# Kernel optimization log

Measured on AMD Instinct MI355X. Metric: run time of the kernel, lower is better.

The kernel has to match this reference:

```python
import math
import jax, jax.numpy as jnp
import numpy as np

N = 65536   # total nodes across episodes
H = 512     # hidden size
B = 4096    # number of episodes / decoding items
M = 32      # max neighbors (padded ragged valid_actions)


def setup_inputs() -> dict:
    key = jax.random.key(0)
    ks = jax.random.split(key, 9)
    s = 1.0 / math.sqrt(H)
    return {
        "h_static": jax.random.normal(ks[0], (N, H), jnp.float32),
        "h_dynamic": jax.random.normal(ks[1], (N, H), jnp.float32),
        "Ws_kvl": jax.random.normal(ks[2], (H, 3 * H), jnp.float32) * s,
        "Wd_kvl": jax.random.normal(ks[3], (H, 3 * H), jnp.float32) * s,
        "Wq": jax.random.normal(ks[4], (H, H), jnp.float32) * s,
        "batch": jax.random.randint(ks[5], (N,), 0, B, jnp.int32),
        "current_nodes": jax.random.randint(ks[6], (B,), 0, N),
        "neigh_idx": jax.random.randint(ks[7], (B, M), 0, N),
        "lengths": jax.random.randint(ks[8], (B,), 0, M + 1),
    }


def reference(h_static, h_dynamic, Ws_kvl, Wd_kvl, Wq, batch, current_nodes, neigh_idx, lengths):
    # precompute(): static KVL projection (full 3H GEMM then chunk, as in torch)
    kvl_s = h_static @ Ws_kvl            # [N, 3H]
    K_s = kvl_s[:, :H]
    # forward_batch(): dynamic projection
    kvl_d = h_dynamic @ Wd_kvl           # [N, 3H]
    K_d = kvl_d[:, :H]
    K = K_s + K_d                        # [N, H]  (V is computed but unused for outputs)
    q = (h_static[current_nodes] + h_dynamic[current_nodes]) @ Wq  # [B, H]

    # padded ragged neighbor attention (replaces the Python loop over B)
    Kn = K[neigh_idx]                                        # [B, M, H]
    compat = jnp.einsum('bmh,bh->bm', Kn, q) / math.sqrt(H)  # [B, M]
    mask = jnp.arange(M)[None, :] < lengths[:, None]         # [B, M]
    NEG = jnp.float32(-1e9)
    logits = jnp.where(mask, compat, NEG)

    # categorical sampling via Gumbel-max (Categorical(logits).sample())
    u = jax.random.uniform(jax.random.key(1), (B, M), jnp.float32, 1e-8, 1.0)
    g = -jnp.log(-jnp.log(u))
    idx = jnp.argmax(logits + g, axis=-1)                    # [B]

    logp = jax.nn.log_softmax(logits, axis=-1)               # [B, M]
    lp = jnp.take_along_axis(logp, idx[:, None], axis=1)[:, 0]
    actions = jnp.take_along_axis(neigh_idx, idx[:, None], axis=1)[:, 0]

    # empty neighbor list -> stay at current node, log_prob 0 (matches torch branch)
    nonempty = lengths > 0
    actions = jnp.where(nonempty, actions, current_nodes)
    lp = jnp.where(nonempty, lp, jnp.float32(0.0))
    return actions, lp
```

## Files before the change

### kernel.cpp

```cpp
#include <hip/hip_runtime.h>
#include <cstdint>
#include <cstddef>

#define HDIM 512
#define NM 32
#define NBATCH 4096
#define NNODE 65536
#define CAP 16

typedef float v4f __attribute__((ext_vector_type(4)));

__device__ __forceinline__ unsigned rotl32(unsigned x, unsigned d) {
  return (x << d) | (x >> (32u - d));
}

__device__ __forceinline__ void threefry2x32(unsigned& x0, unsigned& x1) {
  const unsigned ks0 = 0u, ks1 = 1u, ks2 = 0x1BD11BDBu;
  x0 += ks0; x1 += ks1;
#define TF_RND(r) { x0 += x1; x1 = rotl32(x1, (r)); x1 ^= x0; }
  TF_RND(13) TF_RND(15) TF_RND(26) TF_RND(6)
  x0 += ks1; x1 += ks2 + 1u;
  TF_RND(17) TF_RND(29) TF_RND(16) TF_RND(24)
  x0 += ks2; x1 += ks0 + 2u;
  TF_RND(13) TF_RND(15) TF_RND(26) TF_RND(6)
  x0 += ks0; x1 += ks1 + 3u;
  TF_RND(17) TF_RND(29) TF_RND(16) TF_RND(24)
  x0 += ks1; x1 += ks2 + 4u;
  TF_RND(13) TF_RND(15) TF_RND(26) TF_RND(6)
  x0 += ks2; x1 += ks0 + 5u;
#undef TF_RND
}

__global__ __launch_bounds__(256) void zero_cnt(int* __restrict__ cnt,
                                                int* __restrict__ ovf_cnt) {
  const int t = blockIdx.x * 256 + threadIdx.x;
  ((int4*)cnt)[t] = make_int4(0, 0, 0, 0);
  if (t == 0) *ovf_cnt = 0;
}

__global__ __launch_bounds__(256) void b1_and_index(
    const float* __restrict__ Ws, const float* __restrict__ Wd,
    const float* __restrict__ Wq, float* __restrict__ M2T,
    const int* __restrict__ neigh, const int* __restrict__ lens,
    int* __restrict__ cnt, int* __restrict__ bucket,
    int* __restrict__ ovf_cnt, int* __restrict__ ovf_list) {
  const int bid = blockIdx.x;
  const int tid = threadIdx.x;
  if (bid >= 512) {
    const int t = (bid - 512) * 256 + tid;
    const int b = t >> 5, m = t & 31;
    if (m < lens[b]) {
      const int n = neigh[t];
      const int slot = atomicAdd(&cnt[n], 1);
      if (slot < CAP) bucket[n * CAP + slot] = t;
      else { const int o = atomicAdd(ovf_cnt, 1); ovf_list[o] = t; }
    }
    return;
  }
  constexpr int BK = 32, LDT = 36;
  __shared__ float Ast[BK][LDT];
  __shared__ float Bst[BK][LDT];
  const int rt = bid >> 4;
  const int ct = bid & 15;
  const int row0 = rt * 32;
  const int col0 = ct * 32;
  const float* Abase = (row0 < 512) ? Ws : Wd;
  const int arow0 = (row0 < 512) ? row0 : row0 - 512;
  const int tx = tid & 15, ty = tid >> 4;
  const int lr = tid >> 3;
  const int lc = (tid & 7) * 4;
  float acc[2][2] = {};
  for (int k0 = 0; k0 < 512; k0 += BK) {
    const float4 va = *(const float4*)(Abase + (size_t)(arow0 + lr) * 1536 + k0 + lc);
    const float4 vb = *(const float4*)(Wq + (size_t)(col0 + lr) * 512 + k0 + lc);
    Ast[lc + 0][lr] = va.x; Ast[lc + 1][lr] = va.y;
    Ast[lc + 2][lr] = va.z; Ast[lc + 3][lr] = va.w;
    Bst[lc + 0][lr] = vb.x; Bst[lc + 1][lr] = vb.y;
    Bst[lc + 2][lr] = vb.z; Bst[lc + 3][lr] = vb.w;
    __syncthreads();
#pragma unroll
    for (int k = 0; k < BK; ++k) {
      const float a0 = Ast[k][ty * 2], a1 = Ast[k][ty * 2 + 1];
      const float b0 = Bst[k][tx * 2], b1 = Bst[k][tx * 2 + 1];
      acc[0][0] += a0 * b0; acc[0][1] += a0 * b1;
      acc[1][0] += a1 * b0; acc[1][1] += a1 * b1;
    }
    __syncthreads();
  }
#pragma unroll
  for (int i = 0; i < 2; ++i) {
    float2 o;
    o.x = acc[i][0]; o.y = acc[i][1];
    *(float2*)(M2T + (size_t)(row0 + ty * 2 + i) * 512 + col0 + tx * 2) = o;
  }
}

__global__ __launch_bounds__(256) void gemm_v(const float* __restrict__ hs,
                                              const float* __restrict__ hd,
                                              const int* __restrict__ cur,
                                              const float* __restrict__ Bm,
                                              float* __restrict__ C) {
  __shared__ __align__(16) char smem[51200];
  float* As = (float*)smem;
  float* Bs = (float*)(smem + 33792);
  float* mg = (float*)smem;

  const int tid = threadIdx.x;
  const int team = tid >> 7;
  const int lt = tid & 127;
  const int swz = (blockIdx.x & 7) * 64 + (blockIdx.x >> 3);
  const int row0 = (swz >> 4) * 128;
  const int col0 = (swz & 15) * 64;
  const int tx = tid & 7;
  const int ty = (tid >> 3) & 15;
  const int r0 = lt >> 3;
  const int cq = (lt & 7) * 4;
  const int kb = team * 256;
  const int aoff = team * 4224;
  const int boff = team * 2176;

  size_t na[8];
#pragma unroll
  for (int p = 0; p < 8; ++p)
    na[p] = (size_t)cur[row0 + r0 + 16 * p] * HDIM + kb + cq;
  const float* bbase = Bm + (size_t)(col0 + r0) * 512 + kb + cq;

  float acc[8][8] = {};
#pragma unroll 1
  for (int t = 0; t < 8; ++t) {
    const int k0 = t * 32;
    float4 va[8], vd[8], vb[4];
#pragma unroll
    for (int p = 0; p < 8; ++p) {
      va[p] = *(const float4*)(hs + na[p] + k0);
      vd[p] = *(const float4*)(hd + na[p] + k0);
    }
#pragma unroll
    for (int p = 0; p < 4; ++p)
      vb[p] = *(const float4*)(bbase + p * (16 * 512) + k0);
    __syncthreads();
#pragma unroll
    for (int p = 0; p < 8; ++p) {
      const int r = r0 + 16 * p;
      As[aoff + (cq + 0) * 132 + r] = va[p].x + vd[p].x;
      As[aoff + (cq + 1) * 132 + r] = va[p].y + vd[p].y;
      As[aoff + (cq + 2) * 132 + r] = va[p].z + vd[p].z;
      As[aoff + (cq + 3) * 132 + r] = va[p].w + vd[p].w;
    }
#pragma unroll
    for (int p = 0; p < 4; ++p) {
      const int r = r0 + 16 * p;
      Bs[boff + (cq + 0) * 68 + r] = vb[p].x;
      Bs[boff + (cq + 1) * 68 + r] = vb[p].y;
      Bs[boff + (cq + 2) * 68 + r] = vb[p].z;
      Bs[boff + (cq + 3) * 68 + r] = vb[p].w;
    }
    __syncthreads();
#pragma unroll
    for (int k = 0; k < 32; ++k) {
      const float4 a0 = *(const float4*)&As[aoff + k * 132 + ty * 8];
      const float4 a1 = *(const float4*)&As[aoff + k * 132 + ty * 8 + 4];
      const float4 b0 = *(const float4*)&Bs[boff + k * 68 + tx * 8];
      const float4 b1 = *(const float4*)&Bs[boff + k * 68 + tx * 8 + 4];
      const float a[8] = {a0.x, a0.y, a0.z, a0.w, a1.x, a1.y, a1.z, a1.w};
      const float bb[8] = {b0.x, b0.y, b0.z, b0.w, b1.x, b1.y, b1.z, b1.w};
#pragma unroll
      for (int i = 0; i < 8; ++i)
#pragma unroll
        for (int j = 0; j < 8; ++j) acc[i][j] += a[i] * bb[j];
    }
  }
  __syncthreads();
  if (team == 1) {
#pragma unroll
    for (int i = 0; i < 8; ++i)
#pragma unroll
      for (int j = 0; j < 8; ++j)
        mg[lt * 65 + i * 8 + j] = acc[i][j];
  }
  __syncthreads();
  if (team == 0) {
#pragma unroll
    for (int i = 0; i < 8; ++i) {
#pragma unroll
      for (int j = 0; j < 8; ++j)
        acc[i][j] = acc[i][j] + mg[lt * 65 + i * 8 + j];
      float* cp = C + (size_t)(row0 + ty * 8 + i) * 1024 + col0 + tx * 8;
      float4 o0, o1;
      o0.x = acc[i][0]; o0.y = acc[i][1]; o0.z = acc[i][2]; o0.w = acc[i][3];
      o1.x = acc[i][4]; o1.y = acc[i][5]; o1.z = acc[i][6]; o1.w = acc[i][7];
      *(float4*)cp = o0;
      *(float4*)(cp + 4) = o1;
    }
  }
}

__global__ __launch_bounds__(256) void stream_compat(
    const float* __restrict__ hs, const float* __restrict__ hd,
    const float* __restrict__ V, const int* __restrict__ cnt,
    const int* __restrict__ bucket, const int* __restrict__ ovf_cnt,
    const int* __restrict__ ovf_list, const int* __restrict__ neigh,
    float* __restrict__ compat) {
  const int n = blockIdx.x * 4 + (threadIdx.x >> 6);
  const int lane = threadIdx.x & 63;
  const int c = cnt[n];
  if (c != 0) {
    const v4f* a4 = (const v4f*)(hs + (size_t)n * HDIM);
    const v4f* c4 = (const v4f*)(hd + (size_t)n * HDIM);
    const v4f a0 = __builtin_nontemporal_load(a4 + lane * 2);
    const v4f a1 = __builtin_nontemporal_load(a4 + lane * 2 + 1);
    const v4f b0 = __builtin_nontemporal_load(c4 + lane * 2);
    const v4f b1 = __builtin_nontemporal_load(c4 + lane * 2 + 1);
    const int cc = (c < CAP) ? c : CAP;
    for (int e = 0; e < cc; ++e) {
      const int t = bucket[n * CAP + e];
      const int b = t >> 5;
      const float4* vrow = (const float4*)(V + (size_t)b * (2 * HDIM));
      const float4 w0 = vrow[lane * 2], w1 = vrow[lane * 2 + 1];
      const float4 u0 = vrow[128 + lane * 2], u1 = vrow[128 + lane * 2 + 1];
      float acc = a0.x * w0.x + a0.y * w0.y + a0.z * w0.z + a0.w * w0.w
                + a1.x * w1.x + a1.y * w1.y + a1.z * w1.z + a1.w * w1.w
                + b0.x * u0.x + b0.y * u0.y + b0.z * u0.z + b0.w * u0.w
                + b1.x * u1.x + b1.y * u1.y + b1.z * u1.z + b1.w * u1.w;
#pragma unroll
      for (int off = 32; off >= 1; off >>= 1) acc += __shfl_xor(acc, off);
      if (lane == 0) compat[t] = acc;
    }
  }
  if (blockIdx.x < 32) {
    const int nw = *ovf_cnt;
    for (int e = blockIdx.x * 4 + (threadIdx.x >> 6); e < nw; e += 128) {
      const int t = ovf_list[e];
      const int b = t >> 5;
      const int nn = neigh[t];
      const float4* a4 = (const float4*)(hs + (size_t)nn * HDIM);
      const float4* c4 = (const float4*)(hd + (size_t)nn * HDIM);
      const float4 a0 = a4[lane * 2], a1 = a4[lane * 2 + 1];
      const float4 b0 = c4[lane * 2], b1 = c4[lane * 2 + 1];
      const float4* vrow = (const float4*)(V + (size_t)b * (2 * HDIM));
      const float4 w0 = vrow[lane * 2], w1 = vrow[lane * 2 + 1];
      const float4 u0 = vrow[128 + lane * 2], u1 = vrow[128 + lane * 2 + 1];
      float acc = a0.x * w0.x + a0.y * w0.y + a0.z * w0.z + a0.w * w0.w
                + a1.x * w1.x + a1.y * w1.y + a1.z * w1.z + a1.w * w1.w
                + b0.x * u0.x + b0.y * u0.y + b0.z * u0.z + b0.w * u0.w
                + b1.x * u1.x + b1.y * u1.y + b1.z * u1.z + b1.w * u1.w;
#pragma unroll
      for (int off = 32; off >= 1; off >>= 1) acc += __shfl_xor(acc, off);
      if (lane == 0) compat[t] = acc;
    }
  }
}

__global__ __launch_bounds__(256) void finalize_kernel(
    const float* __restrict__ compat, const int* __restrict__ neigh,
    const int* __restrict__ lengths, const int* __restrict__ cur,
    float* __restrict__ out) {
  const int b = blockIdx.x * 4 + (threadIdx.x >> 6);
  const int tid = threadIdx.x & 63;
  const int len = lengths[b];
  const bool valid = tid < NM;
  const float NEGMAX = -3.402823466e38f;
  float logit = NEGMAX;
  if (valid) {
    const float cm = compat[b * NM + tid] / 22.62741699796952f;
    logit = (tid < len) ? cm : -1e9f;
  }
  float z = NEGMAX;
  int zi = 1 << 20;
  if (valid) {
    const unsigned i_lo = (unsigned)b * 32u + (unsigned)tid;
    unsigned x0 = 0u;
    unsigned x1 = i_lo;
    threefry2x32(x0, x1);
    const unsigned bits = x0 ^ x1;
    const float fu = __uint_as_float((bits >> 9) | 0x3f800000u) - 1.0f;
    const float uu = fmaxf(1e-8f, fu + 1e-8f);
    const float g = -logf(-logf(uu));
    z = logit + g;
    zi = tid;
  }
#pragma unroll
  for (int off = 32; off >= 1; off >>= 1) {
    const float oz = __shfl_xor(z, off);
    const int oi = __shfl_xor(zi, off);
    if (oz > z || (oz == z && oi < zi)) { z = oz; zi = oi; }
  }
  float ml = logit;
#pragma unroll
  for (int off = 32; off >= 1; off >>= 1) ml = fmaxf(ml, __shfl_xor(ml, off));
  float ex = valid ? expf(logit - ml) : 0.f;
#pragma unroll
  for (int off = 32; off >= 1; off >>= 1) ex += __shfl_xor(ex, off);
  const float lsel = __shfl(logit, zi);
  if (tid == 0) {
    float lp = lsel - ml - logf(ex);
    int act = neigh[b * NM + zi];
    if (len <= 0) { act = cur[b]; lp = 0.f; }
    out[b] = (float)act;
    out[NBATCH + b] = lp;
  }
}

extern "C" void kernel_launch(void* const* d_in, const int* in_sizes, int n_in,
                              void* d_out, int out_size, void* d_ws, size_t ws_size,
                              hipStream_t stream) {
  const float* hs = (const float*)d_in[0];
  const float* hd = (const float*)d_in[1];
  const float* Ws = (const float*)d_in[2];
  const float* Wd = (const float*)d_in[3];
  const float* Wq = (const float*)d_in[4];
  const int* cur = (const int*)d_in[6];
  const int* neigh = (const int*)d_in[7];
  const int* lens = (const int*)d_in[8];
  float* out = (float*)d_out;

  char* ws = (char*)d_ws;
  size_t off = 0;
  int* cnt = (int*)(ws + off);        off += (size_t)NNODE * 4;
  int* ovf_cnt = (int*)(ws + off);    off += 256;
  int* bucket = (int*)(ws + off);     off += (size_t)NNODE * CAP * 4;
  int* ovf_list = (int*)(ws + off);   off += (size_t)NBATCH * NM * 4;
  float* compat = (float*)(ws + off); off += (size_t)NBATCH * NM * 4;
  float* M2T = (float*)(ws + off);    off += (size_t)1024 * 512 * 4;
  float* V = (float*)(ws + off);      off += (size_t)NBATCH * 1024 * 4;

  hipLaunchKernelGGL(zero_cnt, dim3(64), dim3(256), 0, stream, cnt, ovf_cnt);
  hipLaunchKernelGGL(b1_and_index, dim3(512 + NBATCH * NM / 256), dim3(256), 0, stream,
                     Ws, Wd, Wq, M2T, neigh, lens, cnt, bucket, ovf_cnt, ovf_list);
  hipLaunchKernelGGL(gemm_v, dim3(512), dim3(256), 0, stream, hs, hd, cur, M2T, V);
  hipLaunchKernelGGL(stream_compat, dim3(NNODE / 4), dim3(256), 0, stream,
                     hs, hd, V, cnt, bucket, ovf_cnt, ovf_list, neigh, compat);
  hipLaunchKernelGGL(finalize_kernel, dim3(NBATCH / 4), dim3(256), 0, stream,
                     compat, neigh, lens, cur, out);
}
```

Before: 155.8 us.

## Retile gemm_v to 128x32 tiles with 128 threads and drop split-K merge

```diff
diff --git a/kernel.cpp b/kernel.cpp
--- a/kernel.cpp
+++ b/kernel.cpp
@@ -95,103 +95,73 @@
   }
 }
 
-__global__ __launch_bounds__(256) void gemm_v(const float* __restrict__ hs,
+__global__ __launch_bounds__(128) void gemm_v(const float* __restrict__ hs,
                                               const float* __restrict__ hd,
                                               const int* __restrict__ cur,
                                               const float* __restrict__ Bm,
                                               float* __restrict__ C) {
-  __shared__ __align__(16) char smem[51200];
-  float* As = (float*)smem;
-  float* Bs = (float*)(smem + 33792);
-  float* mg = (float*)smem;
-
+  constexpr int LDA = 132, LDB = 36;
+  __shared__ float As[32][LDA];
+  __shared__ float Bs[32][LDB];
   const int tid = threadIdx.x;
-  const int team = tid >> 7;
-  const int lt = tid & 127;
-  const int swz = (blockIdx.x & 7) * 64 + (blockIdx.x >> 3);
-  const int row0 = (swz >> 4) * 128;
-  const int col0 = (swz & 15) * 64;
+  const int swz = (int)(blockIdx.x & 7) * 128 + (int)(blockIdx.x >> 3);
+  const int row0 = (swz >> 5) * 128;
+  const int col0 = (swz & 31) * 32;
   const int tx = tid & 7;
-  const int ty = (tid >> 3) & 15;
-  const int r0 = lt >> 3;
-  const int cq = (lt & 7) * 4;
-  const int kb = team * 256;
-  const int aoff = team * 4224;
-  const int boff = team * 2176;
+  const int ty = tid >> 3;
+  const int r0 = tid >> 3;
+  const int cq = (tid & 7) * 4;
 
   size_t na[8];
 #pragma unroll
   for (int p = 0; p < 8; ++p)
-    na[p] = (size_t)cur[row0 + r0 + 16 * p] * HDIM + kb + cq;
-  const float* bbase = Bm + (size_t)(col0 + r0) * 512 + kb + cq;
-
-  float acc[8][8] = {};
+    na[p] = (size_t)cur[row0 + r0 + 16 * p] * HDIM + cq;
+  const float* bb0 = Bm + (size_t)(col0 + r0) * 512 + cq;
+
+  float acc[8][4] = {};
 #pragma unroll 1
-  for (int t = 0; t < 8; ++t) {
+  for (int t = 0; t < 16; ++t) {
     const int k0 = t * 32;
-    float4 va[8], vd[8], vb[4];
+    float4 va[8], vd[8], vb0, vb1;
 #pragma unroll
     for (int p = 0; p < 8; ++p) {
       va[p] = *(const float4*)(hs + na[p] + k0);
       vd[p] = *(const float4*)(hd + na[p] + k0);
     }
-#pragma unroll
-    for (int p = 0; p < 4; ++p)
-      vb[p] = *(const float4*)(bbase + p * (16 * 512) + k0);
+    vb0 = *(const float4*)(bb0 + k0);
+    vb1 = *(const float4*)(bb0 + 16 * 512 + k0);
     __syncthreads();
 #pragma unroll
     for (int p = 0; p < 8; ++p) {
       const int r = r0 + 16 * p;
-      As[aoff + (cq + 0) * 132 + r] = va[p].x + vd[p].x;
-      As[aoff + (cq + 1) * 132 + r] = va[p].y + vd[p].y;
-      As[aoff + (cq + 2) * 132 + r] = va[p].z + vd[p].z;
-      As[aoff + (cq + 3) * 132 + r] = va[p].w + vd[p].w;
-    }
-#pragma unroll
-    for (int p = 0; p < 4; ++p) {
-      const int r = r0 + 16 * p;
-      Bs[boff + (cq + 0) * 68 + r] = vb[p].x;
-      Bs[boff + (cq + 1) * 68 + r] = vb[p].y;
-      Bs[boff + (cq + 2) * 68 + r] = vb[p].z;
-      Bs[boff + (cq + 3) * 68 + r] = vb[p].w;
-    }
+      As[cq + 0][r] = va[p].x + vd[p].x;
+      As[cq + 1][r] = va[p].y + vd[p].y;
+      As[cq + 2][r] = va[p].z + vd[p].z;
+      As[cq + 3][r] = va[p].w + vd[p].w;
+    }
+    Bs[cq + 0][r0] = vb0.x; Bs[cq + 1][r0] = vb0.y;
+    Bs[cq + 2][r0] = vb0.z; Bs[cq + 3][r0] = vb0.w;
+    Bs[cq + 0][r0 + 16] = vb1.x; Bs[cq + 1][r0 + 16] = vb1.y;
+    Bs[cq + 2][r0 + 16] = vb1.z; Bs[cq + 3][r0 + 16] = vb1.w;
     __syncthreads();
 #pragma unroll
     for (int k = 0; k < 32; ++k) {
-      const float4 a0 = *(const float4*)&As[aoff + k * 132 + ty * 8];
-      const float4 a1 = *(const float4*)&As[aoff + k * 132 + ty * 8 + 4];
-      const float4 b0 = *(const float4*)&Bs[boff + k * 68 + tx * 8];
-      const float4 b1 = *(const float4*)&Bs[boff + k * 68 + tx * 8 + 4];
+      const float4 a0 = *(const float4*)&As[k][ty * 8];
+      const float4 a1 = *(const float4*)&As[k][ty * 8 + 4];
+      const float4 b4 = *(const float4*)&Bs[k][tx * 4];
       const float a[8] = {a0.x, a0.y, a0.z, a0.w, a1.x, a1.y, a1.z, a1.w};
-      const float bb[8] = {b0.x, b0.y, b0.z, b0.w, b1.x, b1.y, b1.z, b1.w};
+      const float bb[4] = {b4.x, b4.y, b4.z, b4.w};
 #pragma unroll
       for (int i = 0; i < 8; ++i)
 #pragma unroll
-        for (int j = 0; j < 8; ++j) acc[i][j] += a[i] * bb[j];
-    }
-  }
-  __syncthreads();
-  if (team == 1) {
-#pragma unroll
-    for (int i = 0; i < 8; ++i)
-#pragma unroll
-      for (int j = 0; j < 8; ++j)
-        mg[lt * 65 + i * 8 + j] = acc[i][j];
-  }
-  __syncthreads();
-  if (team == 0) {
-#pragma unroll
-    for (int i = 0; i < 8; ++i) {
-#pragma unroll
-      for (int j = 0; j < 8; ++j)
-        acc[i][j] = acc[i][j] + mg[lt * 65 + i * 8 + j];
-      float* cp = C + (size_t)(row0 + ty * 8 + i) * 1024 + col0 + tx * 8;
-      float4 o0, o1;
-      o0.x = acc[i][0]; o0.y = acc[i][1]; o0.z = acc[i][2]; o0.w = acc[i][3];
-      o1.x = acc[i][4]; o1.y = acc[i][5]; o1.z = acc[i][6]; o1.w = acc[i][7];
-      *(float4*)cp = o0;
-      *(float4*)(cp + 4) = o1;
-    }
+        for (int j = 0; j < 4; ++j) acc[i][j] += a[i] * bb[j];
+    }
+  }
+#pragma unroll
+  for (int i = 0; i < 8; ++i) {
+    float4 o;
+    o.x = acc[i][0]; o.y = acc[i][1]; o.z = acc[i][2]; o.w = acc[i][3];
+    *(float4*)(C + (size_t)(row0 + ty * 8 + i) * 1024 + col0 + tx * 4) = o;
   }
 }
 
@@ -327,7 +297,7 @@
   hipLaunchKernelGGL(zero_cnt, dim3(64), dim3(256), 0, stream, cnt, ovf_cnt);
   hipLaunchKernelGGL(b1_and_index, dim3(512 + NBATCH * NM / 256), dim3(256), 0, stream,
                      Ws, Wd, Wq, M2T, neigh, lens, cnt, bucket, ovf_cnt, ovf_list);
-  hipLaunchKernelGGL(gemm_v, dim3(512), dim3(256), 0, stream, hs, hd, cur, M2T, V);
+  hipLaunchKernelGGL(gemm_v, dim3(1024), dim3(128), 0, stream, hs, hd, cur, M2T, V);
   hipLaunchKernelGGL(stream_compat, dim3(NNODE / 4), dim3(256), 0, stream,
                      hs, hd, V, cnt, bucket, ovf_cnt, ovf_list, neigh, compat);
   hipLaunchKernelGGL(finalize_kernel, dim3(NBATCH / 4), dim3(256), 0, stream,
```

Measured after the change: 171.5 us. +10.1%, slower.
